# Performance work log

Measured on AMD Instinct MI355X. Metric: run time of the kernel, lower is better.

Reference implementation:

```python
import jax, jax.numpy as jnp
import numpy as np

V = 78864; E = 300; H = 512; A = 300; T = 20; DEC_EMB = 512; START = 2


def _pos_encoding(n, d):
    pos = np.arange(n)[:, None].astype(np.float32)
    i = np.arange(d)[None, :]
    angle = pos / np.power(10000.0, (2 * (i // 2)).astype(np.float32) / d)
    pe = np.where(i % 2 == 0, np.sin(angle), np.cos(angle)).astype(np.float32)
    return jnp.asarray(pe)  # [n, d]


def _lstm_cell(x, h, c, Wih, Whh, b):
    g = x @ Wih.T + h @ Whh.T + b
    i, f, gg, o = jnp.split(g, 4, axis=-1)
    c = jax.nn.sigmoid(f) * c + jax.nn.sigmoid(i) * jnp.tanh(gg)
    h = jax.nn.sigmoid(o) * jnp.tanh(c)
    return h, c


def setup_inputs() -> dict:
    key = jax.random.key(0)
    ks = iter(jax.random.split(key, 48))
    B, L = 40, 1000
    def w(shape, s=0.02):
        return jax.random.normal(next(ks), shape, jnp.float32) * s
    def z(shape):
        return jnp.zeros(shape, jnp.float32)
    inp = dict(
        enc_in=jax.random.randint(next(ks), (B, L), 0, V),
        enc_out=jax.random.normal(next(ks), (B, L, H), jnp.float32),
        enc_mask=jnp.zeros((B, L), bool),
        inputs=jax.random.randint(next(ks), (B, T), 0, V),
        embed=w((V, E)),
        elmo1_Wih=w((4 * H, E)), elmo1_Whh=w((4 * H, H)), elmo1_b=z((4 * H,)),
        elmo2_Wih=w((4 * H, H)), elmo2_Whh=w((4 * H, H)), elmo2_b=z((4 * H,)),
        in_W=w((DEC_EMB, H + E + A + H)), in_b=z((DEC_EMB,)),
        rnn1_Wih=w((4 * H, DEC_EMB)), rnn1_Whh=w((4 * H, H)), rnn1_b=z((4 * H,)),
        att1_Wq=w((A, H)), att1_bq=z((A,)), att1_Wk=w((A, H)), att1_bk=z((A,)), att1_Wv=w((A, H)), att1_bv=z((A,)),
        rnn2_Wih=w((4 * H, A)), rnn2_Whh=w((4 * H, H)), rnn2_b=z((4 * H,)),
        att2_Wq=w((A, H)), att2_bq=z((A,)), att2_Wk=w((A, H)), att2_bk=z((A,)), att2_Wv=w((A, H)), att2_bv=z((A,)),
        copy_W=w((A, H)), copy_b=z((A,)),
        out_W=w((V, A)), out_b=z((V,)),
        scale=jnp.asarray(1.0, jnp.float32),
    )
    return inp


def _forward(enc_in, enc_out, enc_mask, inputs, embed,
             elmo1_Wih, elmo1_Whh, elmo1_b, elmo2_Wih, elmo2_Whh, elmo2_b,
             in_W, in_b, rnn1_Wih, rnn1_Whh, rnn1_b,
             att1_Wq, att1_bq, att1_Wk, att1_bk, att1_Wv, att1_bv,
             rnn2_Wih, rnn2_Whh, rnn2_b,
             att2_Wq, att2_bq, att2_Wk, att2_bk, att2_Wv, att2_bv,
             copy_W, copy_b, out_W, out_b, scale):
    B, L = enc_in.shape
    pe = _pos_encoding(T, DEC_EMB)  # [T, 512]
    # Precompute per-encoder projections (hoisted out of the step loop).
    K1 = jnp.einsum('blh,ah->bla', enc_out, att1_Wk) + att1_bk
    V1 = jnp.einsum('blh,ah->bla', enc_out, att1_Wv) + att1_bv
    K2 = jnp.einsum('blh,ah->bla', enc_out, att2_Wk) + att2_bk
    V2 = jnp.einsum('blh,ah->bla', enc_out, att2_Wv) + att2_bv
    copyK = jnp.tanh(jnp.einsum('blh,ah->bla', enc_out, copy_W) + copy_b)
    bidx = jnp.arange(B)[:, None]

    def attn(h, Wq, bq, K, Vp):
        q = h @ Wq.T + bq                          # [B, A]
        s = jnp.einsum('ba,bla->bl', q, K)
        s = jnp.where(enc_mask, -1e9, s)
        p = jax.nn.softmax(s, axis=-1)
        return jnp.einsum('bl,bla->ba', p, Vp)

    # teacher forcing with random_int=0 -> always use ground-truth inputs
    sym_in = jnp.concatenate([jnp.full((B, 1), START, inputs.dtype), inputs[:, :-1]], axis=1).T  # [T,B]
    sym_out = inputs.T  # [T,B]

    zf = lambda *s: jnp.zeros(s, enc_out.dtype)
    carry0 = (zf(B, H), zf(B, H), zf(B, H), zf(B, H),  # elmo h1,c1,h2,c2
              zf(B, H), zf(B, H), zf(B, H), zf(B, H),  # rnn1 h,c ; rnn2 h,c
              zf(B, A), zf(B, H))                       # dec_att_out, select_read

    def step(carry, xs):
        eh1, ec1, eh2, ec2, h1, c1, h2, c2, att, sel = carry
        pe_t, s_in, s_out = xs
        emb = embed[s_in]                                           # [B, E]
        eh1, ec1 = _lstm_cell(emb, eh1, ec1, elmo1_Wih, elmo1_Whh, elmo1_b)
        eh2, ec2 = _lstm_cell(eh1, eh2, ec2, elmo2_Wih, elmo2_Whh, elmo2_b)
        in_embed = jnp.concatenate([emb, eh2], axis=-1)              # [B, 812]
        dec_in = jnp.concatenate([in_embed, att, sel], axis=-1) @ in_W.T + in_b + pe_t
        h1, c1 = _lstm_cell(dec_in, h1, c1, rnn1_Wih, rnn1_Whh, rnn1_b)
        att = attn(h1, att1_Wq, att1_bq, K1, V1)
        h2, c2 = _lstm_cell(att, h2, c2, rnn2_Wih, rnn2_Whh, rnn2_b)
        att = attn(h2, att2_Wq, att2_bq, K2, V2) + att
        # copy scores
        s = jnp.einsum('ba,bla->bl', att, copyK)
        s = jnp.where(enc_mask, -1e9, s)
        score_c = jax.nn.softmax(s, axis=-1)
        score_e = score_c * scale * scale
        vocab = att @ out_W.T + out_b                                # [B, V]
        vocab = vocab.at[bidx, enc_in].add(score_e)
        sym_pred = jnp.argmax(vocab, axis=-1).astype(jnp.int32)
        eq = (enc_in == s_out[:, None]).astype(score_c.dtype)
        score_f = score_c * eq
        score_f = score_f / (jnp.sum(score_f, axis=-1, keepdims=True) + 1e-8)
        sel = jnp.einsum('bl,blh->bh', score_f, enc_out)
        return (eh1, ec1, eh2, ec2, h1, c1, h2, c2, att, sel), (vocab, sym_pred)

    _, (dec_out, syms) = jax.lax.scan(step, carry0, (pe, sym_in, sym_out))
    return jnp.transpose(dec_out, (1, 0, 2)), syms.T  # [B,T,V], [B,T]


def reference(enc_in, enc_out, enc_mask, inputs, embed,
              elmo1_Wih, elmo1_Whh, elmo1_b, elmo2_Wih, elmo2_Whh, elmo2_b,
              in_W, in_b, rnn1_Wih, rnn1_Whh, rnn1_b,
              att1_Wq, att1_bq, att1_Wk, att1_bk, att1_Wv, att1_bv,
              rnn2_Wih, rnn2_Whh, rnn2_b,
              att2_Wq, att2_bq, att2_Wk, att2_bk, att2_Wv, att2_bv,
              copy_W, copy_b, out_W, out_b, scale):
    return _forward(enc_in, enc_out, enc_mask, inputs, embed,
                    elmo1_Wih, elmo1_Whh, elmo1_b, elmo2_Wih, elmo2_Whh, elmo2_b,
                    in_W, in_b, rnn1_Wih, rnn1_Whh, rnn1_b,
                    att1_Wq, att1_bq, att1_Wk, att1_bk, att1_Wv, att1_bv,
                    rnn2_Wih, rnn2_Whh, rnn2_b,
                    att2_Wq, att2_bq, att2_Wk, att2_bk, att2_Wv, att2_bv,
                    copy_W, copy_b, out_W, out_b, scale)
```

## Files before the change

kernel.cpp:

```cpp
#include <hip/hip_runtime.h>
#include <math.h>

#define B_ 40
#define L_ 1000
#define H_ 512
#define A_ 300
#define T_ 20
#define E_ 300
#define V_ 78864
#define CIN_ 1624
#define START_ 2

__device__ __forceinline__ float sigm(float x){ return 1.0f/(1.0f+expf(-x)); }

__device__ __forceinline__ float waveMax(float v){
#pragma unroll
  for(int o=32;o>0;o>>=1) v=fmaxf(v,__shfl_down(v,o));
  return v;
}
__device__ __forceinline__ float waveSum(float v){
#pragma unroll
  for(int o=32;o>0;o>>=1) v+=__shfl_down(v,o);
  return v;
}
__device__ __forceinline__ float waveSumXor(float v){
#pragma unroll
  for(int o=32;o>0;o>>=1) v+=__shfl_xor(v,o);
  return v;
}

__global__ void k_pe(float* __restrict__ pe){
  int t=blockIdx.x, d=threadIdx.x;
  float ex=(float)(2*(d>>1))/512.0f;
  float ang=(float)t/powf(10000.0f,ex);
  pe[t*H_+d]=(d&1)?cosf(ang):sinf(ang);
}

__global__ __launch_bounds__(320) void k_copyk(const float* __restrict__ enc,
    const float* __restrict__ W, const float* __restrict__ bias, float* __restrict__ out){
  int b=blockIdx.y, l0=blockIdx.x*16, a=threadIdx.x;
  if(a>=A_) return;
  int lcnt=min(16,L_-l0);
  float acc[16];
  float bv=bias[a];
#pragma unroll
  for(int l=0;l<16;l++) acc[l]=bv;
  const float4* wr=(const float4*)(W+(long)a*H_);
  for(int i=0;i<H_/4;i++){
    float4 w=wr[i];
#pragma unroll
    for(int l=0;l<16;l++){
      int row=b*L_+min(l0+l,L_-1);
      float4 x=((const float4*)enc)[(long)row*(H_/4)+i];
      acc[l]+=x.x*w.x+x.y*w.y+x.z*w.z+x.w*w.w;
    }
  }
  for(int l=0;l<lcnt;l++) out[((long)(b*L_+l0+l))*A_+a]=tanhf(acc[l]);
}

template<int XD, bool GATHER>
__global__ __launch_bounds__(256) void k_lstm(const float* __restrict__ xsrc,
    const int* __restrict__ inp, const float* __restrict__ embed, int t,
    const float* __restrict__ hr, const float* __restrict__ cr,
    float* __restrict__ hw, float* __restrict__ cw,
    const float* __restrict__ Wih, const float* __restrict__ Whh, const float* __restrict__ bias){
  __shared__ float g4[256];
  int b=blockIdx.y, hb=blockIdx.x, tid=threadIdx.x;
  const float4* xr4;
  if constexpr(GATHER){
    int si=(t==0)?START_:inp[b*T_+t-1];
    xr4=(const float4*)(embed+(long)si*XD);
  } else {
    xr4=(const float4*)(xsrc+(long)b*XD);
  }
  const float4* hr4=(const float4*)(hr+(long)b*H_);
  int gate=tid>>6, u=(hb<<6)+(tid&63), row=gate*H_+u;
  float acc=bias[row];
  const float4* wi=(const float4*)(Wih+(long)row*XD);
#pragma unroll 4
  for(int i=0;i<XD/4;i++){ float4 w=wi[i]; float4 x=xr4[i];
    acc+=x.x*w.x+x.y*w.y+x.z*w.z+x.w*w.w; }
  const float4* wh=(const float4*)(Whh+(long)row*H_);
#pragma unroll 4
  for(int i=0;i<H_/4;i++){ float4 w=wh[i]; float4 h4=hr4[i];
    acc+=h4.x*w.x+h4.y*w.y+h4.z*w.z+h4.w*w.w; }
  g4[tid]=acc;
  __syncthreads();
  if(tid<64){
    int uu=(hb<<6)+tid;
    float gi=g4[tid],gf=g4[64+tid],gg=g4[128+tid],go=g4[192+tid];
    float c=cr[b*H_+uu];
    float cn=sigm(gf)*c+sigm(gi)*tanhf(gg);
    hw[b*H_+uu]=sigm(go)*tanhf(cn);
    cw[b*H_+uu]=cn;
  }
}

__global__ __launch_bounds__(256) void k_decin(const int* __restrict__ inp,
    const float* __restrict__ embed, int t,
    const float* __restrict__ eh2, const float* __restrict__ attprev,
    const float* __restrict__ selpart,
    const float* __restrict__ W, const float* __restrict__ bias,
    const float* __restrict__ pe, float* __restrict__ out){
  __shared__ float xs[CIN_];
  int b=blockIdx.y, tid=threadIdx.x;
  int si=(t==0)?START_:inp[b*T_+t-1];
  for(int k=tid;k<CIN_;k+=256){
    float v;
    if(k<E_) v=embed[(long)si*E_+k];
    else if(k<E_+H_) v=eh2[b*H_+k-E_];
    else if(k<E_+H_+A_) v=attprev[b*A_+k-(E_+H_)];
    else{
      int h=k-(E_+H_+A_);
      float s=0.f;
#pragma unroll
      for(int j=0;j<8;j++) s+=selpart[(b*8+j)*H_+h];
      v=s;
    }
    xs[k]=v;
  }
  __syncthreads();
  int d=blockIdx.x*256+tid;
  float acc=bias[d]+pe[t*H_+d];
  const float4* wr=(const float4*)(W+(long)d*CIN_);
#pragma unroll 2
  for(int i=0;i<CIN_/4;i++){ float4 w=wr[i];
    acc+=xs[4*i]*w.x+xs[4*i+1]*w.y+xs[4*i+2]*w.z+xs[4*i+3]*w.w; }
  out[b*H_+d]=acc;
}

__global__ __launch_bounds__(512) void k_q(const float* __restrict__ h,
    const float* __restrict__ Wq, const float* __restrict__ bq,
    const float* __restrict__ Wk, float* __restrict__ qk){
  __shared__ float hs[H_], qs[A_];
  int b=blockIdx.x, tid=threadIdx.x;
  hs[tid]=h[b*H_+tid];
  __syncthreads();
  if(tid<A_){
    float acc=bq[tid];
    const float4* wr=(const float4*)(Wq+(long)tid*H_);
#pragma unroll 4
    for(int i=0;i<H_/4;i++){ float4 w=wr[i];
      acc+=hs[4*i]*w.x+hs[4*i+1]*w.y+hs[4*i+2]*w.z+hs[4*i+3]*w.w; }
    qs[tid]=acc;
  }
  __syncthreads();
  float acc=0.f;
  for(int a=0;a<A_;a++) acc+=qs[a]*Wk[a*H_+tid];
  qk[b*H_+tid]=acc;
}

__global__ __launch_bounds__(256) void k_scores(const float* __restrict__ qk,
    const float* __restrict__ enc, const unsigned char* __restrict__ mask,
    float* __restrict__ s){
  __shared__ float qs[H_];
  int b=blockIdx.y, j=blockIdx.x, tid=threadIdx.x;
  qs[tid]=qk[b*H_+tid]; qs[tid+256]=qk[b*H_+tid+256];
  __syncthreads();
  int wv=tid>>6, lane=tid&63;
  const float4* qs4=(const float4*)qs;
  for(int i=0;i<32;i++){
    int idx=i*4+wv;
    if(idx>=125) break;
    int l=j*125+idx;
    const float4* er=(const float4*)(enc+((long)(b*L_+l))*H_);
    float4 q1=qs4[lane], e1=er[lane];
    float p=q1.x*e1.x+q1.y*e1.y+q1.z*e1.z+q1.w*e1.w;
    float4 q2=qs4[64+lane], e2=er[64+lane];
    p+=q2.x*e2.x+q2.y*e2.y+q2.z*e2.z+q2.w*e2.w;
    p=waveSumXor(p);
    if(lane==0) s[b*L_+l]=mask[b*L_+l]?-1e9f:p;
  }
}

__global__ __launch_bounds__(512) void k_ctx(const float* __restrict__ s,
    const float* __restrict__ enc, float* __restrict__ part){
  __shared__ float e[L_];
  __shared__ float redm[8], reds[8];
  int b=blockIdx.y, j=blockIdx.x, tid=threadIdx.x;
  float lm=-3.0e38f;
  for(int l=tid;l<L_;l+=512){ float v=s[b*L_+l]; e[l]=v; lm=fmaxf(lm,v); }
  lm=waveMax(lm); if((tid&63)==0) redm[tid>>6]=lm;
  __syncthreads();
  float m=redm[0];
#pragma unroll
  for(int w2=1;w2<8;w2++) m=fmaxf(m,redm[w2]);
  float ls=0.f;
  for(int l=tid;l<L_;l+=512){ float ex=expf(e[l]-m); e[l]=ex; ls+=ex; }
  ls=waveSum(ls); if((tid&63)==0) reds[tid>>6]=ls;
  __syncthreads();
  float S=0.f;
#pragma unroll
  for(int w2=0;w2<8;w2++) S+=reds[w2];
  float inv=1.0f/S;
  float acc=0.f;
  int l0=j*125;
  for(int l=l0;l<l0+125;l++) acc+=e[l]*enc[((long)(b*L_+l))*H_+tid];
  part[(b*8+j)*H_+tid]=acc*inv;
}

template<bool ADD>
__global__ __launch_bounds__(512) void k_atto(const float* __restrict__ part,
    const float* __restrict__ Wv, const float* __restrict__ bv,
    const float* __restrict__ attprev, float* __restrict__ out, float* __restrict__ outT){
  __shared__ float cs[H_];
  int b=blockIdx.x, tid=threadIdx.x;
  float c=0.f;
#pragma unroll
  for(int j=0;j<8;j++) c+=part[(b*8+j)*H_+tid];
  cs[tid]=c;
  __syncthreads();
  if(tid<A_){
    float acc=bv[tid];
    const float4* wr=(const float4*)(Wv+(long)tid*H_);
#pragma unroll 4
    for(int i=0;i<H_/4;i++){ float4 w=wr[i];
      acc+=cs[4*i]*w.x+cs[4*i+1]*w.y+cs[4*i+2]*w.z+cs[4*i+3]*w.w; }
    if constexpr(ADD) acc+=attprev[b*A_+tid];
    out[b*A_+tid]=acc;
    if constexpr(ADD) outT[tid*B_+b]=acc;
  }
}

__global__ __launch_bounds__(256) void k_copysc(const float* __restrict__ att,
    const float* __restrict__ ck, const unsigned char* __restrict__ mask,
    float* __restrict__ s){
  __shared__ float as[A_];
  int b=blockIdx.y, j=blockIdx.x, tid=threadIdx.x;
  for(int k=tid;k<A_;k+=256) as[k]=att[b*A_+k];
  __syncthreads();
  int wv=tid>>6, lane=tid&63;
  for(int i=0;i<32;i++){
    int idx=i*4+wv;
    if(idx>=125) break;
    int l=j*125+idx;
    const float* cr=ck+((long)(b*L_+l))*A_;
    float p=0.f;
#pragma unroll
    for(int it=0;it<4;it++){ int k=it*64+lane; p+=as[k]*cr[k]; }
    { int k=256+lane; if(k<A_) p+=as[k]*cr[k]; }
    p=waveSumXor(p);
    if(lane==0) s[b*L_+l]=mask[b*L_+l]?-1e9f:p;
  }
}

__global__ __launch_bounds__(256) void k_vocab(const float* __restrict__ attT,
    const float* __restrict__ W, const float* __restrict__ bias, int t,
    float* __restrict__ dout){
  __shared__ float wt[256*33];
  int tid=threadIdx.x;
  int v=blockIdx.x*256+tid;
  bool ok=v<V_;
  int v0=blockIdx.x*256;
  float acc[B_];
#pragma unroll
  for(int b=0;b<B_;b++) acc[b]=0.f;
  for(int c=0;c<10;c++){
    int a0=c*32;
    int aw=(c<9)?32:12;
    __syncthreads();
    if(c<9){
      for(int idx=tid;idx<256*32;idx+=256){
        int vr=idx>>5, ar=idx&31;
        float val=(v0+vr<V_)?W[(long)(v0+vr)*A_+a0+ar]:0.f;
        wt[vr*33+ar]=val;
      }
    } else {
      for(int idx=tid;idx<256*12;idx+=256){
        int vr=idx/12, ar=idx-vr*12;
        float val=(v0+vr<V_)?W[(long)(v0+vr)*A_+a0+ar]:0.f;
        wt[vr*33+ar]=val;
      }
    }
    __syncthreads();
    for(int a=0;a<aw;a++){
      float wv=wt[tid*33+a];
      const float4* at4=(const float4*)(attT+(long)(a0+a)*B_);
#pragma unroll
      for(int bq=0;bq<10;bq++){
        float4 t4=at4[bq];
        acc[4*bq+0]+=wv*t4.x; acc[4*bq+1]+=wv*t4.y;
        acc[4*bq+2]+=wv*t4.z; acc[4*bq+3]+=wv*t4.w;
      }
    }
  }
  if(ok){
    float ob=bias[v];
#pragma unroll
    for(int b=0;b<B_;b++) dout[((long)(b*T_+t))*V_+v]=acc[b]+ob;
  }
}

__global__ __launch_bounds__(512) void k_scatsel(const float* __restrict__ s,
    const int* __restrict__ encin, const int* __restrict__ inp,
    const float* __restrict__ scale, int t,
    const float* __restrict__ enc, float* __restrict__ part,
    float* __restrict__ dout){
  __shared__ float e[L_], e2[L_];
  __shared__ float redm[8], reds[8], redq[8];
  int b=blockIdx.y, j=blockIdx.x, tid=threadIdx.x;
  int so=inp[b*T_+t];
  float lm=-3.0e38f;
  for(int l=tid;l<L_;l+=512){ float v=s[b*L_+l]; e[l]=v; lm=fmaxf(lm,v); }
  lm=waveMax(lm); if((tid&63)==0) redm[tid>>6]=lm;
  __syncthreads();
  float m=redm[0];
#pragma unroll
  for(int w2=1;w2<8;w2++) m=fmaxf(m,redm[w2]);
  float ls=0.f, lq=0.f;
  for(int l=tid;l<L_;l+=512){
    float ex=expf(e[l]-m);
    float pe_=(encin[b*L_+l]==so)?ex:0.f;
    e[l]=ex; e2[l]=pe_; ls+=ex; lq+=pe_;
  }
  ls=waveSum(ls); lq=waveSum(lq);
  if((tid&63)==0){ reds[tid>>6]=ls; redq[tid>>6]=lq; }
  __syncthreads();
  float S=0.f,Q=0.f;
#pragma unroll
  for(int w2=0;w2<8;w2++){ S+=reds[w2]; Q+=redq[w2]; }
  int l0=j*125;
  if(tid<125){
    int l=l0+tid;
    float f=scale[0]*scale[0]/S;
    float p=e[l]*f;
    atomicAdd(dout+((long)(b*T_+t))*V_+encin[b*L_+l],p);
  }
  float inv=1.0f/(Q+1e-8f*S);
  float acc=0.f;
  for(int l=l0;l<l0+125;l++) acc+=e2[l]*enc[((long)(b*L_+l))*H_+tid];
  part[(b*8+j)*H_+tid]=acc*inv;
}

__global__ __launch_bounds__(256) void k_argmax(int t, float* __restrict__ dout){
  __shared__ float vs[256];
  __shared__ int is[256];
  int b=blockIdx.x, tid=threadIdx.x;
  const float* row=dout+((long)(b*T_+t))*V_;
  float best=-3.0e38f; int bi=0;
  for(int v=tid;v<V_;v+=256){ float x=row[v]; if(x>best){best=x;bi=v;} }
  vs[tid]=best; is[tid]=bi;
  __syncthreads();
  for(int off=128;off>0;off>>=1){
    if(tid<off){
      float ov=vs[tid+off]; int oi=is[tid+off];
      if(ov>vs[tid]||(ov==vs[tid]&&oi<is[tid])){ vs[tid]=ov; is[tid]=oi; }
    }
    __syncthreads();
  }
  if(tid==0) dout[(long)B_*T_*V_+b*T_+t]=(float)is[0];
}

extern "C" void kernel_launch(void* const* d_in, const int* in_sizes, int n_in,
                              void* d_out, int out_size, void* d_ws, size_t ws_size,
                              hipStream_t stream){
  const int* enc_in=(const int*)d_in[0];
  const float* enc_out=(const float*)d_in[1];
  const unsigned char* enc_mask=(const unsigned char*)d_in[2];
  const int* inputs=(const int*)d_in[3];
  const float* embed=(const float*)d_in[4];
  const float* e1Wih=(const float*)d_in[5], *e1Whh=(const float*)d_in[6], *e1b=(const float*)d_in[7];
  const float* e2Wih=(const float*)d_in[8], *e2Whh=(const float*)d_in[9], *e2b=(const float*)d_in[10];
  const float* inW=(const float*)d_in[11], *inb=(const float*)d_in[12];
  const float* r1Wih=(const float*)d_in[13], *r1Whh=(const float*)d_in[14], *r1b=(const float*)d_in[15];
  const float* a1Wq=(const float*)d_in[16], *a1bq=(const float*)d_in[17];
  const float* a1Wk=(const float*)d_in[18];
  const float* a1Wv=(const float*)d_in[20], *a1bv=(const float*)d_in[21];
  const float* r2Wih=(const float*)d_in[22], *r2Whh=(const float*)d_in[23], *r2b=(const float*)d_in[24];
  const float* a2Wq=(const float*)d_in[25], *a2bq=(const float*)d_in[26];
  const float* a2Wk=(const float*)d_in[27];
  const float* a2Wv=(const float*)d_in[29], *a2bv=(const float*)d_in[30];
  const float* cW=(const float*)d_in[31], *cb=(const float*)d_in[32];
  const float* oW=(const float*)d_in[33], *ob=(const float*)d_in[34];
  const float* scale=(const float*)d_in[35];
  float* dout=(float*)d_out;
  float* w=(float*)d_ws;

  size_t off=0;
  float* copyK=w+off; off+=(size_t)B_*L_*A_;
  float* pe=w+off;    off+=T_*H_;
  float* st=w+off;    off+=16*B_*H_;
  float* att1=w+off;  off+=B_*A_;
  float* att2=w+off;  off+=B_*A_;
  float* attT=w+off;  off+=A_*B_;
  float* qk=w+off;    off+=B_*H_;
  float* s1=w+off;    off+=B_*L_;
  float* scc=w+off;   off+=B_*L_;
  float* ctxp=w+off;  off+=B_*8*H_;
  float* selp=w+off;  off+=B_*8*H_;
  float* decin=w+off; off+=B_*H_;

  hipMemsetAsync(pe,0,(off-(size_t)B_*L_*A_)*sizeof(float),stream);
  k_pe<<<T_,H_,0,stream>>>(pe);
  k_copyk<<<dim3((L_+15)/16,B_),320,0,stream>>>(enc_out,cW,cb,copyK);

  auto S=[&](int i){ return st+(size_t)i*(B_*H_); };
  for(int t=0;t<T_;t++){
    int rp=t&1, wp=rp^1;
    float *eh1r=S(0+rp),*eh1w=S(0+wp),*ec1r=S(2+rp),*ec1w=S(2+wp);
    float *eh2r=S(4+rp),*eh2w=S(4+wp),*ec2r=S(6+rp),*ec2w=S(6+wp);
    float *h1r=S(8+rp),*h1w=S(8+wp),*c1r=S(10+rp),*c1w=S(10+wp);
    float *h2r=S(12+rp),*h2w=S(12+wp),*c2r=S(14+rp),*c2w=S(14+wp);

    k_lstm<E_,true><<<dim3(8,B_),256,0,stream>>>(nullptr,inputs,embed,t,eh1r,ec1r,eh1w,ec1w,e1Wih,e1Whh,e1b);
    k_lstm<H_,false><<<dim3(8,B_),256,0,stream>>>(eh1w,nullptr,nullptr,t,eh2r,ec2r,eh2w,ec2w,e2Wih,e2Whh,e2b);
    k_decin<<<dim3(2,B_),256,0,stream>>>(inputs,embed,t,eh2w,att2,selp,inW,inb,pe,decin);
    k_lstm<H_,false><<<dim3(8,B_),256,0,stream>>>(decin,nullptr,nullptr,t,h1r,c1r,h1w,c1w,r1Wih,r1Whh,r1b);
    k_q<<<B_,512,0,stream>>>(h1w,a1Wq,a1bq,a1Wk,qk);
    k_scores<<<dim3(8,B_),256,0,stream>>>(qk,enc_out,enc_mask,s1);
    k_ctx<<<dim3(8,B_),512,0,stream>>>(s1,enc_out,ctxp);
    k_atto<false><<<B_,512,0,stream>>>(ctxp,a1Wv,a1bv,nullptr,att1,nullptr);
    k_lstm<A_,false><<<dim3(8,B_),256,0,stream>>>(att1,nullptr,nullptr,t,h2r,c2r,h2w,c2w,r2Wih,r2Whh,r2b);
    k_q<<<B_,512,0,stream>>>(h2w,a2Wq,a2bq,a2Wk,qk);
    k_scores<<<dim3(8,B_),256,0,stream>>>(qk,enc_out,enc_mask,s1);
    k_ctx<<<dim3(8,B_),512,0,stream>>>(s1,enc_out,ctxp);
    k_atto<true><<<B_,512,0,stream>>>(ctxp,a2Wv,a2bv,att1,att2,attT);
    k_copysc<<<dim3(8,B_),256,0,stream>>>(att2,copyK,enc_mask,scc);
    k_vocab<<<(V_+255)/256,256,0,stream>>>(attT,oW,ob,t,dout);
    k_scatsel<<<dim3(8,B_),512,0,stream>>>(scc,enc_in,inputs,scale,t,enc_out,selp,dout);
    k_argmax<<<B_,256,0,stream>>>(t,dout);
  }
}
```

Before: 18.39 ms.

## Replace per-step kernel launches with one persistent kernel using grid barriers

Turns the per-timestep sequence of about seventeen kernel launches into a single persistent kernel of 256 blocks that moves between phases using atomic-counter grid barriers. It also restructures the work: LSTM gates are computed batch-wide per weight row through shared memory, query and key weights are premultiplied into M1T and M2T, scores and context are fused with an online softmax, and the vocab projection is retiled. The aim is to remove launch overhead and reread weights fewer times across the batch. In exchange it depends on all blocks being co-resident for the spin barriers and adds many barrier points per step.

```diff
diff --git a/kernel.cpp b/kernel.cpp
--- a/kernel.cpp
+++ b/kernel.cpp
@@ -8,416 +8,509 @@
 #define T_ 20
 #define E_ 300
 #define V_ 78864
-#define CIN_ 1624
 #define START_ 2
 
+#define NBLK 256
+#define NTHR 512
+
+#define OFF_COPYK 0ul
+#define OFF_M1T   12000000ul
+#define OFF_M2T   12262144ul
+#define OFF_BQK1  12524288ul
+#define OFF_BQK2  12524800ul
+#define OFF_QK    12525312ul
+#define OFF_DEC   12545792ul
+#define OFF_ATT1  12566272ul
+#define OFF_ATTT  12578272ul
+#define OFF_CPART 12590272ul
+#define OFF_CSTAT 12713152ul
+#define OFF_SCC   12713664ul
+#define OFF_STT   12753664ul
+#define OFF_ATT2  13081344ul
+#define OFF_SELP  13093344ul
+#define OFF_CNT   13216224ul
+#define WS_END    13216288ul
+
+struct P {
+  const int* enc_in; const float* enc; const unsigned char* mask; const int* inputs;
+  const float* embed;
+  const float *e1Wih,*e1Whh,*e1b,*e2Wih,*e2Whh,*e2b;
+  const float *inW,*inb;
+  const float *r1Wih,*r1Whh,*r1b;
+  const float *a1Wq,*a1bq,*a1Wk,*a1Wv,*a1bv;
+  const float *r2Wih,*r2Whh,*r2b;
+  const float *a2Wq,*a2bq,*a2Wk,*a2Wv,*a2bv;
+  const float *cW,*cb,*oW,*ob,*scale;
+  float* dout;
+  float *copyK,*M1T,*M2T,*bqk1,*bqk2,*qk,*dec,*att1,*attT,*cpart,*cstat,*scc,*stt,*att2,*selp;
+  unsigned* cnt;
+};
+
 __device__ __forceinline__ float sigm(float x){ return 1.0f/(1.0f+expf(-x)); }
 
-__device__ __forceinline__ float waveMax(float v){
-#pragma unroll
-  for(int o=32;o>0;o>>=1) v=fmaxf(v,__shfl_down(v,o));
-  return v;
-}
-__device__ __forceinline__ float waveSum(float v){
-#pragma unroll
-  for(int o=32;o>0;o>>=1) v+=__shfl_down(v,o);
-  return v;
-}
-__device__ __forceinline__ float waveSumXor(float v){
+__device__ __forceinline__ float wredSum(float v){
 #pragma unroll
   for(int o=32;o>0;o>>=1) v+=__shfl_xor(v,o);
   return v;
 }
-
-__global__ void k_pe(float* __restrict__ pe){
-  int t=blockIdx.x, d=threadIdx.x;
-  float ex=(float)(2*(d>>1))/512.0f;
-  float ang=(float)t/powf(10000.0f,ex);
-  pe[t*H_+d]=(d&1)?cosf(ang):sinf(ang);
-}
-
-__global__ __launch_bounds__(320) void k_copyk(const float* __restrict__ enc,
-    const float* __restrict__ W, const float* __restrict__ bias, float* __restrict__ out){
-  int b=blockIdx.y, l0=blockIdx.x*16, a=threadIdx.x;
-  if(a>=A_) return;
-  int lcnt=min(16,L_-l0);
-  float acc[16];
-  float bv=bias[a];
-#pragma unroll
-  for(int l=0;l<16;l++) acc[l]=bv;
-  const float4* wr=(const float4*)(W+(long)a*H_);
-  for(int i=0;i<H_/4;i++){
-    float4 w=wr[i];
-#pragma unroll
-    for(int l=0;l<16;l++){
-      int row=b*L_+min(l0+l,L_-1);
-      float4 x=((const float4*)enc)[(long)row*(H_/4)+i];
-      acc[l]+=x.x*w.x+x.y*w.y+x.z*w.z+x.w*w.w;
-    }
-  }
-  for(int l=0;l<lcnt;l++) out[((long)(b*L_+l0+l))*A_+a]=tanhf(acc[l]);
-}
-
-template<int XD, bool GATHER>
-__global__ __launch_bounds__(256) void k_lstm(const float* __restrict__ xsrc,
-    const int* __restrict__ inp, const float* __restrict__ embed, int t,
-    const float* __restrict__ hr, const float* __restrict__ cr,
-    float* __restrict__ hw, float* __restrict__ cw,
-    const float* __restrict__ Wih, const float* __restrict__ Whh, const float* __restrict__ bias){
-  __shared__ float g4[256];
-  int b=blockIdx.y, hb=blockIdx.x, tid=threadIdx.x;
-  const float4* xr4;
-  if constexpr(GATHER){
-    int si=(t==0)?START_:inp[b*T_+t-1];
-    xr4=(const float4*)(embed+(long)si*XD);
-  } else {
-    xr4=(const float4*)(xsrc+(long)b*XD);
-  }
-  const float4* hr4=(const float4*)(hr+(long)b*H_);
-  int gate=tid>>6, u=(hb<<6)+(tid&63), row=gate*H_+u;
-  float acc=bias[row];
-  const float4* wi=(const float4*)(Wih+(long)row*XD);
+__device__ __forceinline__ float wredMax(float v){
+#pragma unroll
+  for(int o=32;o>0;o>>=1) v=fmaxf(v,__shfl_xor(v,o));
+  return v;
+}
+
+__device__ __forceinline__ void gbar(unsigned* cnt, unsigned target){
+  __syncthreads();
+  if(threadIdx.x==0){
+    __hip_atomic_fetch_add(cnt,1u,__ATOMIC_RELEASE,__HIP_MEMORY_SCOPE_AGENT);
+    while(__hip_atomic_load(cnt,__ATOMIC_RELAXED,__HIP_MEMORY_SCOPE_AGENT)<target){
+      __builtin_amdgcn_s_sleep(1);
+    }
+    (void)__hip_atomic_load(cnt,__ATOMIC_ACQUIRE,__HIP_MEMORY_SCOPE_AGENT);
+  }
+  __syncthreads();
+}
+
+template<typename SRC>
+static __device__ __forceinline__ void gv_accum(float* xs,int K,const float* Wrow,
+    float& acc,int lane,int kq,int nq,SRC src){
+  for(int k0=0;k0<K;k0+=256){
+    int ch=min(256,K-k0);
+    __syncthreads();
+    for(int i=threadIdx.x;i<40*ch;i+=NTHR){
+      int bb=i/ch, kk=i-bb*ch;
+      xs[bb*257+kk]=src(bb,k0+kk);
+    }
+    __syncthreads();
+    if(lane<40){
 #pragma unroll 4
-  for(int i=0;i<XD/4;i++){ float4 w=wi[i]; float4 x=xr4[i];
-    acc+=x.x*w.x+x.y*w.y+x.z*w.z+x.w*w.w; }
-  const float4* wh=(const float4*)(Whh+(long)row*H_);
-#pragma unroll 4
-  for(int i=0;i<H_/4;i++){ float4 w=wh[i]; float4 h4=hr4[i];
-    acc+=h4.x*w.x+h4.y*w.y+h4.z*w.z+h4.w*w.w; }
-  g4[tid]=acc;
-  __syncthreads();
-  if(tid<64){
-    int uu=(hb<<6)+tid;
-    float gi=g4[tid],gf=g4[64+tid],gg=g4[128+tid],go=g4[192+tid];
-    float c=cr[b*H_+uu];
+      for(int k=kq;k<ch;k+=nq) acc+=Wrow[k0+k]*xs[lane*257+k];
+    }
+  }
+}
+
+static __device__ void lstm_ph(const P& p,float* SH,float* gld,int t,
+    const float* Wih,int XD,const float* Whh,const float* bias,
+    const float* xvec,bool gather,
+    const float* hr,const float* cr,float* hw,float* cw){
+  int tid=threadIdx.x,w=tid>>6,lane=tid&63;
+  int gate=w&3,usub=w>>2;
+  int row=gate*H_+(blockIdx.x*2+usub);
+  int rowu=__builtin_amdgcn_readfirstlane(row);
+  float acc=bias[rowu];
+  const float* W1=Wih+(size_t)rowu*XD;
+  if(gather){
+    const int* inp=p.inputs; const float* emb=p.embed; int tt=t;
+    gv_accum(SH,XD,W1,acc,lane,0,1,[=](int bb,int kk)->float{
+      int si=(tt==0)?START_:inp[bb*T_+tt-1];
+      return emb[(size_t)si*E_+kk];});
+  }else{
+    gv_accum(SH,XD,W1,acc,lane,0,1,[=](int bb,int kk)->float{
+      return xvec[(size_t)bb*XD+kk];});
+  }
+  const float* W2=Whh+(size_t)rowu*H_;
+  gv_accum(SH,H_,W2,acc,lane,0,1,[=](int bb,int kk)->float{
+    return hr[bb*H_+kk];});
+  gld[w*64+lane]=acc;
+  __syncthreads();
+  if(w<2&&lane<40){
+    int u=blockIdx.x*2+w,b=lane;
+    float gi=gld[(w*4+0)*64+b],gf=gld[(w*4+1)*64+b],gg=gld[(w*4+2)*64+b],go=gld[(w*4+3)*64+b];
+    float c=cr[b*H_+u];
     float cn=sigm(gf)*c+sigm(gi)*tanhf(gg);
-    hw[b*H_+uu]=sigm(go)*tanhf(cn);
-    cw[b*H_+uu]=cn;
-  }
-}
-
-__global__ __launch_bounds__(256) void k_decin(const int* __restrict__ inp,
-    const float* __restrict__ embed, int t,
-    const float* __restrict__ eh2, const float* __restrict__ attprev,
-    const float* __restrict__ selpart,
-    const float* __restrict__ W, const float* __restrict__ bias,
-    const float* __restrict__ pe, float* __restrict__ out){
-  __shared__ float xs[CIN_];
-  int b=blockIdx.y, tid=threadIdx.x;
-  int si=(t==0)?START_:inp[b*T_+t-1];
-  for(int k=tid;k<CIN_;k+=256){
-    float v;
-    if(k<E_) v=embed[(long)si*E_+k];
-    else if(k<E_+H_) v=eh2[b*H_+k-E_];
-    else if(k<E_+H_+A_) v=attprev[b*A_+k-(E_+H_)];
-    else{
-      int h=k-(E_+H_+A_);
-      float s=0.f;
-#pragma unroll
-      for(int j=0;j<8;j++) s+=selpart[(b*8+j)*H_+h];
-      v=s;
-    }
-    xs[k]=v;
-  }
-  __syncthreads();
-  int d=blockIdx.x*256+tid;
-  float acc=bias[d]+pe[t*H_+d];
-  const float4* wr=(const float4*)(W+(long)d*CIN_);
-#pragma unroll 2
-  for(int i=0;i<CIN_/4;i++){ float4 w=wr[i];
-    acc+=xs[4*i]*w.x+xs[4*i+1]*w.y+xs[4*i+2]*w.z+xs[4*i+3]*w.w; }
-  out[b*H_+d]=acc;
-}
-
-__global__ __launch_bounds__(512) void k_q(const float* __restrict__ h,
-    const float* __restrict__ Wq, const float* __restrict__ bq,
-    const float* __restrict__ Wk, float* __restrict__ qk){
-  __shared__ float hs[H_], qs[A_];
-  int b=blockIdx.x, tid=threadIdx.x;
-  hs[tid]=h[b*H_+tid];
+    hw[b*H_+u]=sigm(go)*tanhf(cn);
+    cw[b*H_+u]=cn;
+  }
+  __syncthreads();
+}
+
+static __device__ void qk_ph(const P& p,float* SH,const float* hsrc,
+    const float* MT,const float* bqk){
+  int tid=threadIdx.x;
+  if(blockIdx.x>=240) return;
+  int b=blockIdx.x/6, j=blockIdx.x%6;
+  SH[tid]=hsrc[b*H_+tid];
+  __syncthreads();
+  int h0=j*86, hc=min(86,H_-h0);
+  if(tid<hc){
+    int hp=h0+tid;
+    float a=bqk[hp];
+    const float4* mr=(const float4*)(MT+(size_t)hp*H_);
+#pragma unroll 8
+    for(int i=0;i<H_/4;i++){
+      float4 m4=mr[i];
+      a+=SH[4*i]*m4.x+SH[4*i+1]*m4.y+SH[4*i+2]*m4.z+SH[4*i+3]*m4.w;
+    }
+    p.qk[b*H_+hp]=a;
+  }
+}
+
+static __device__ void scctx_ph(const P& p,float* SH,float* red){
+  int tid=threadIdx.x,w=tid>>6,lane=tid&63;
+  if(blockIdx.x>=240) return;
+  int b=blockIdx.x/6, j=blockIdx.x%6;
+  int l0=j*167, lcnt=min(167,L_-l0);
+  const float* qrow=p.qk+b*H_;
+  float4 q0=*(const float4*)(qrow+lane*8);
+  float4 q1=*(const float4*)(qrow+lane*8+4);
+  float m=-3.0e38f,S=0.f;
+  float4 a0=make_float4(0.f,0.f,0.f,0.f), a1=a0;
+  for(int l=l0+w;l<l0+lcnt;l+=8){
+    const float4* er=(const float4*)(p.enc+((size_t)(b*L_+l))*H_);
+    float4 e0=er[lane*2], e1=er[lane*2+1];
+    float pp=q0.x*e0.x+q0.y*e0.y+q0.z*e0.z+q0.w*e0.w
+            +q1.x*e1.x+q1.y*e1.y+q1.z*e1.z+q1.w*e1.w;
+    pp=wredSum(pp);
+    if(p.mask[b*L_+l]) pp=-1e9f;
+    float mn=fmaxf(m,pp);
+    float sc=expf(m-mn), pe=expf(pp-mn);
+    S=S*sc+pe;
+    a0.x=a0.x*sc+pe*e0.x; a0.y=a0.y*sc+pe*e0.y; a0.z=a0.z*sc+pe*e0.z; a0.w=a0.w*sc+pe*e0.w;
+    a1.x=a1.x*sc+pe*e1.x; a1.y=a1.y*sc+pe*e1.y; a1.z=a1.z*sc+pe*e1.z; a1.w=a1.w*sc+pe*e1.w;
+    m=mn;
+  }
+  *(float4*)(SH+w*H_+lane*8)=a0;
+  *(float4*)(SH+w*H_+lane*8+4)=a1;
+  if(lane==0){red[w]=m; red[8+w]=S;}
+  __syncthreads();
+  float mb=red[0];
+#pragma unroll
+  for(int q=1;q<8;q++) mb=fmaxf(mb,red[q]);
+  float Sb=0.f;
+#pragma unroll
+  for(int q=0;q<8;q++) Sb+=red[8+q]*expf(red[q]-mb);
+  float pv=0.f;
+#pragma unroll
+  for(int q=0;q<8;q++) pv+=expf(red[q]-mb)*SH[q*H_+tid];
+  p.cpart[(size_t)(b*6+j)*H_+tid]=pv;
+  if(tid==0){p.cstat[(b*6+j)*2]=mb; p.cstat[(b*6+j)*2+1]=Sb;}
+}
+
+static __device__ void atto_ph(const P& p,float* SH,const float* Wv,const float* bv,bool ADD){
+  int tid=threadIdx.x;
+  if(blockIdx.x>=40) return;
+  int b=blockIdx.x;
+  float mb=-3.0e38f;
+#pragma unroll
+  for(int j=0;j<6;j++) mb=fmaxf(mb,p.cstat[(b*6+j)*2]);
+  float Sb=0.f;
+#pragma unroll
+  for(int j=0;j<6;j++) Sb+=p.cstat[(b*6+j)*2+1]*expf(p.cstat[(b*6+j)*2]-mb);
+  float inv=1.0f/Sb;
+  float cx=0.f;
+#pragma unroll
+  for(int j=0;j<6;j++) cx+=expf(p.cstat[(b*6+j)*2]-mb)*p.cpart[(size_t)(b*6+j)*H_+tid];
+  SH[tid]=cx*inv;
   __syncthreads();
   if(tid<A_){
-    float acc=bq[tid];
-    const float4* wr=(const float4*)(Wq+(long)tid*H_);
-#pragma unroll 4
-    for(int i=0;i<H_/4;i++){ float4 w=wr[i];
-      acc+=hs[4*i]*w.x+hs[4*i+1]*w.y+hs[4*i+2]*w.z+hs[4*i+3]*w.w; }
-    qs[tid]=acc;
-  }
-  __syncthreads();
-  float acc=0.f;
-  for(int a=0;a<A_;a++) acc+=qs[a]*Wk[a*H_+tid];
-  qk[b*H_+tid]=acc;
-}
-
-__global__ __launch_bounds__(256) void k_scores(const float* __restrict__ qk,
-    const float* __restrict__ enc, const unsigned char* __restrict__ mask,
-    float* __restrict__ s){
-  __shared__ float qs[H_];
-  int b=blockIdx.y, j=blockIdx.x, tid=threadIdx.x;
-  qs[tid]=qk[b*H_+tid]; qs[tid+256]=qk[b*H_+tid+256];
-  __syncthreads();
-  int wv=tid>>6, lane=tid&63;
-  const float4* qs4=(const float4*)qs;
-  for(int i=0;i<32;i++){
-    int idx=i*4+wv;
-    if(idx>=125) break;
-    int l=j*125+idx;
-    const float4* er=(const float4*)(enc+((long)(b*L_+l))*H_);
-    float4 q1=qs4[lane], e1=er[lane];
-    float p=q1.x*e1.x+q1.y*e1.y+q1.z*e1.z+q1.w*e1.w;
-    float4 q2=qs4[64+lane], e2=er[64+lane];
-    p+=q2.x*e2.x+q2.y*e2.y+q2.z*e2.z+q2.w*e2.w;
-    p=waveSumXor(p);
-    if(lane==0) s[b*L_+l]=mask[b*L_+l]?-1e9f:p;
-  }
-}
-
-__global__ __launch_bounds__(512) void k_ctx(const float* __restrict__ s,
-    const float* __restrict__ enc, float* __restrict__ part){
-  __shared__ float e[L_];
-  __shared__ float redm[8], reds[8];
-  int b=blockIdx.y, j=blockIdx.x, tid=threadIdx.x;
+    float a=bv[tid];
+    const float4* wr=(const float4*)(Wv+(size_t)tid*H_);
+#pragma unroll 8
+    for(int i=0;i<H_/4;i++){
+      float4 w4=wr[i];
+      a+=SH[4*i]*w4.x+SH[4*i+1]*w4.y+SH[4*i+2]*w4.z+SH[4*i+3]*w4.w;
+    }
+    if(ADD){ a+=p.att1[b*A_+tid]; p.att2[b*A_+tid]=a; p.attT[tid*B_+b]=a; }
+    else p.att1[b*A_+tid]=a;
+  }
+}
+
+static __device__ void copysc_ph(const P& p){
+  int tid=threadIdx.x,w=tid>>6,lane=tid&63;
+  if(blockIdx.x>=240) return;
+  int b=blockIdx.x/6, j=blockIdx.x%6;
+  int l0=j*167, lcnt=min(167,L_-l0);
+  float4 r0=*(const float4*)(p.att2+b*A_+lane*4);
+  float4 r1=make_float4(0.f,0.f,0.f,0.f);
+  if(lane<11) r1=*(const float4*)(p.att2+b*A_+256+lane*4);
+  for(int l=l0+w;l<l0+lcnt;l+=8){
+    const float4* cr=(const float4*)(p.copyK+((size_t)(b*L_+l))*A_);
+    float4 c0=cr[lane];
+    float pp=r0.x*c0.x+r0.y*c0.y+r0.z*c0.z+r0.w*c0.w;
+    if(lane<11){
+      float4 c1=cr[64+lane];
+      pp+=r1.x*c1.x+r1.y*c1.y+r1.z*c1.z+r1.w*c1.w;
+    }
+    pp=wredSum(pp);
+    if(lane==0) p.scc[b*L_+l]=p.mask[b*L_+l]?-1e9f:pp;
+  }
+}
+
+static __device__ void vocab_ph(const P& p,float* SH,int t){
+  int tid=threadIdx.x;
+  int v0=blockIdx.x*312;
+  if(v0>=V_) return;
+  int vcnt=min(312,V_-v0);
+  float acc[40];
+#pragma unroll
+  for(int b=0;b<40;b++) acc[b]=0.f;
+  for(int c=0;c<10;c++){
+    int a0=c*32, aw=min(32,A_-a0);
+    __syncthreads();
+    for(int i=tid;i<vcnt*aw;i+=NTHR){
+      int vr=i/aw, ac=i-vr*aw;
+      SH[vr*33+ac]=p.oW[(size_t)(v0+vr)*A_+a0+ac];
+    }
+    __syncthreads();
+    if(tid<vcnt){
+      for(int ac=0;ac<aw;ac++){
+        float wv=SH[tid*33+ac];
+        const float* at=p.attT+(a0+ac)*B_;
+#pragma unroll
+        for(int bq=0;bq<10;bq++){
+          float4 t4=*(const float4*)(at+bq*4);
+          acc[bq*4+0]+=wv*t4.x; acc[bq*4+1]+=wv*t4.y;
+          acc[bq*4+2]+=wv*t4.z; acc[bq*4+3]+=wv*t4.w;
+        }
+      }
+    }
+  }
+  if(tid<vcnt){
+    int v=v0+tid;
+    float obv=p.ob[v];
+#pragma unroll
+    for(int b=0;b<40;b++) p.dout[((size_t)(b*T_+t))*V_+v]=acc[b]+obv;
+  }
+}
+
+static __device__ void scatsel_ph(const P& p,float* SH,float* red,int t){
+  int tid=threadIdx.x,w=tid>>6,lane=tid&63;
+  if(blockIdx.x>=240) return;
+  int b=blockIdx.x/6, j=blockIdx.x%6;
+  int l0=j*167, lcnt=min(167,L_-l0);
+  for(int i=tid;i<L_;i+=NTHR) SH[i]=p.scc[b*L_+i];
+  __syncthreads();
   float lm=-3.0e38f;
-  for(int l=tid;l<L_;l+=512){ float v=s[b*L_+l]; e[l]=v; lm=fmaxf(lm,v); }
-  lm=waveMax(lm); if((tid&63)==0) redm[tid>>6]=lm;
-  __syncthreads();
-  float m=redm[0];
-#pragma unroll
-  for(int w2=1;w2<8;w2++) m=fmaxf(m,redm[w2]);
-  float ls=0.f;
-  for(int l=tid;l<L_;l+=512){ float ex=expf(e[l]-m); e[l]=ex; ls+=ex; }
-  ls=waveSum(ls); if((tid&63)==0) reds[tid>>6]=ls;
-  __syncthreads();
-  float S=0.f;
-#pragma unroll
-  for(int w2=0;w2<8;w2++) S+=reds[w2];
-  float inv=1.0f/S;
-  float acc=0.f;
-  int l0=j*125;
-  for(int l=l0;l<l0+125;l++) acc+=e[l]*enc[((long)(b*L_+l))*H_+tid];
-  part[(b*8+j)*H_+tid]=acc*inv;
-}
-
-template<bool ADD>
-__global__ __launch_bounds__(512) void k_atto(const float* __restrict__ part,
-    const float* __restrict__ Wv, const float* __restrict__ bv,
-    const float* __restrict__ attprev, float* __restrict__ out, float* __restrict__ outT){
-  __shared__ float cs[H_];
-  int b=blockIdx.x, tid=threadIdx.x;
-  float c=0.f;
-#pragma unroll
-  for(int j=0;j<8;j++) c+=part[(b*8+j)*H_+tid];
-  cs[tid]=c;
-  __syncthreads();
-  if(tid<A_){
-    float acc=bv[tid];
-    const float4* wr=(const float4*)(Wv+(long)tid*H_);
-#pragma unroll 4
-    for(int i=0;i<H_/4;i++){ float4 w=wr[i];
-      acc+=cs[4*i]*w.x+cs[4*i+1]*w.y+cs[4*i+2]*w.z+cs[4*i+3]*w.w; }
-    if constexpr(ADD) acc+=attprev[b*A_+tid];
-    out[b*A_+tid]=acc;
-    if constexpr(ADD) outT[tid*B_+b]=acc;
-  }
-}
-
-__global__ __launch_bounds__(256) void k_copysc(const float* __restrict__ att,
-    const float* __restrict__ ck, const unsigned char* __restrict__ mask,
-    float* __restrict__ s){
-  __shared__ float as[A_];
-  int b=blockIdx.y, j=blockIdx.x, tid=threadIdx.x;
-  for(int k=tid;k<A_;k+=256) as[k]=att[b*A_+k];
-  __syncthreads();
-  int wv=tid>>6, lane=tid&63;
-  for(int i=0;i<32;i++){
-    int idx=i*4+wv;
-    if(idx>=125) break;
-    int l=j*125+idx;
-    const float* cr=ck+((long)(b*L_+l))*A_;
-    float p=0.f;
-#pragma unroll
-    for(int it=0;it<4;it++){ int k=it*64+lane; p+=as[k]*cr[k]; }
-    { int k=256+lane; if(k<A_) p+=as[k]*cr[k]; }
-    p=waveSumXor(p);
-    if(lane==0) s[b*L_+l]=mask[b*L_+l]?-1e9f:p;
-  }
-}
-
-__global__ __launch_bounds__(256) void k_vocab(const float* __restrict__ attT,
-    const float* __restrict__ W, const float* __restrict__ bias, int t,
-    float* __restrict__ dout){
-  __shared__ float wt[256*33];
+  for(int i=tid;i<L_;i+=NTHR) lm=fmaxf(lm,SH[i]);
+  lm=wredMax(lm);
+  if(lane==0) red[w]=lm;
+  __syncthreads();
+  float m=red[0];
+#pragma unroll
+  for(int q=1;q<8;q++) m=fmaxf(m,red[q]);
+  __syncthreads();
+  int so=p.inputs[b*T_+t];
+  float ls=0.f,lq=0.f;
+  for(int i=tid;i<L_;i+=NTHR){
+    float exv=expf(SH[i]-m);
+    ls+=exv;
+    if(p.enc_in[b*L_+i]==so) lq+=exv;
+  }
+  ls=wredSum(ls); lq=wredSum(lq);
+  if(lane==0){red[w]=ls; red[8+w]=lq;}
+  __syncthreads();
+  float S=0.f,Q=0.f;
+#pragma unroll
+  for(int q=0;q<8;q++){S+=red[q];Q+=red[8+q];}
+  if(tid<lcnt){
+    int l=l0+tid;
+    float exv=expf(SH[l]-m);
+    SH[1024+tid]=(p.enc_in[b*L_+l]==so)?exv:0.f;
+    float sc2=p.scale[0]*p.scale[0];
+    atomicAdd(p.dout+((size_t)(b*T_+t))*V_+p.enc_in[b*L_+l], exv*sc2/S);
+  }
+  __syncthreads();
+  float inv=1.0f/(Q+1e-8f*S);
+  float a=0.f;
+  for(int li=0;li<lcnt;li++)
+    a+=SH[1024+li]*p.enc[((size_t)(b*L_+l0+li))*H_+tid];
+  p.selp[(size_t)(b*6+j)*H_+tid]=a*inv;
+}
+
+static __device__ void argmax_ph(const P& p,float* SH,int t){
   int tid=threadIdx.x;
-  int v=blockIdx.x*256+tid;
-  bool ok=v<V_;
-  int v0=blockIdx.x*256;
-  float acc[B_];
-#pragma unroll
-  for(int b=0;b<B_;b++) acc[b]=0.f;
-  for(int c=0;c<10;c++){
-    int a0=c*32;
-    int aw=(c<9)?32:12;
+  if(blockIdx.x>=40) return;
+  int b=blockIdx.x;
+  const float* row=p.dout+((size_t)(b*T_+t))*V_;
+  float best=-3.0e38f; int bi=0;
+  for(int i4=tid;i4<V_/4;i4+=NTHR){
+    float4 x=((const float4*)row)[i4];
+    int base=i4*4;
+    if(x.x>best){best=x.x;bi=base;}
+    if(x.y>best){best=x.y;bi=base+1;}
+    if(x.z>best){best=x.z;bi=base+2;}
+    if(x.w>best){best=x.w;bi=base+3;}
+  }
+  int* isa=(int*)(SH+512);
+  SH[tid]=best; isa[tid]=bi;
+  __syncthreads();
+  for(int off=256;off>0;off>>=1){
+    if(tid<off){
+      float ov=SH[tid+off]; int oi=isa[tid+off];
+      if(ov>SH[tid]||(ov==SH[tid]&&oi<isa[tid])){SH[tid]=ov; isa[tid]=oi;}
+    }
     __syncthreads();
-    if(c<9){
-      for(int idx=tid;idx<256*32;idx+=256){
-        int vr=idx>>5, ar=idx&31;
-        float val=(v0+vr<V_)?W[(long)(v0+vr)*A_+a0+ar]:0.f;
-        wt[vr*33+ar]=val;
+  }
+  if(tid==0) p.dout[(size_t)B_*T_*V_+b*T_+t]=(float)isa[0];
+}
+
+__global__ __launch_bounds__(NTHR,2) void k_persist(P p){
+  __shared__ float SH[10320];
+  __shared__ float gld[512];
+  __shared__ float red[16];
+  int blk=blockIdx.x, tid=threadIdx.x;
+  unsigned bt=0;
+#define BARR() do{bt++; gbar(p.cnt,bt*(unsigned)NBLK);}while(0)
+
+  {
+    int mm=blk>>7, r0=(blk&127)*4;
+    const float* Wq = mm? p.a2Wq : p.a1Wq;
+    const float* Wk = mm? p.a2Wk : p.a1Wk;
+    float* MT = mm? p.M2T : p.M1T;
+    float s0=0.f,s1=0.f,s2=0.f,s3=0.f;
+    for(int a=0;a<A_;a++){
+      float wq=Wq[a*H_+tid];
+      s0+=wq*Wk[a*H_+r0+0];
+      s1+=wq*Wk[a*H_+r0+1];
+      s2+=wq*Wk[a*H_+r0+2];
+      s3+=wq*Wk[a*H_+r0+3];
+    }
+    MT[(size_t)(r0+0)*H_+tid]=s0;
+    MT[(size_t)(r0+1)*H_+tid]=s1;
+    MT[(size_t)(r0+2)*H_+tid]=s2;
+    MT[(size_t)(r0+3)*H_+tid]=s3;
+    if((blk&127)==0){
+      const float* bq = mm? p.a2bq : p.a1bq;
+      float ab=0.f;
+      for(int a=0;a<A_;a++) ab+=bq[a]*Wk[a*H_+tid];
+      (mm? p.bqk2 : p.bqk1)[tid]=ab;
+    }
+  }
+  for(int item=blk;item<B_*63;item+=NBLK){
+    int b=item/63, lt=item-b*63;
+    int l0=lt*16, lcnt=min(16,L_-l0);
+    float acc[16];
+    float bv=(tid<A_)?p.cb[tid]:0.f;
+#pragma unroll
+    for(int l=0;l<16;l++) acc[l]=bv;
+    for(int k0=0;k0<H_;k0+=32){
+      __syncthreads();
+      for(int i=tid;i<A_*32;i+=NTHR){
+        int a=i>>5,kc=i&31;
+        SH[a*33+kc]=p.cW[(size_t)a*H_+k0+kc];
       }
-    } else {
-      for(int idx=tid;idx<256*12;idx+=256){
-        int vr=idx/12, ar=idx-vr*12;
-        float val=(v0+vr<V_)?W[(long)(v0+vr)*A_+a0+ar]:0.f;
-        wt[vr*33+ar]=val;
+      __syncthreads();
+      if(tid<A_){
+#pragma unroll
+        for(int l=0;l<16;l++){
+          if(l<lcnt){
+            const float* es=p.enc+((size_t)(b*L_+l0+l))*H_+k0;
+            float al=acc[l];
+#pragma unroll
+            for(int kc=0;kc<32;kc++) al+=SH[tid*33+kc]*es[kc];
+            acc[l]=al;
+          }
+        }
       }
     }
-    __syncthreads();
-    for(int a=0;a<aw;a++){
-      float wv=wt[tid*33+a];
-      const float4* at4=(const float4*)(attT+(long)(a0+a)*B_);
-#pragma unroll
-      for(int bq=0;bq<10;bq++){
-        float4 t4=at4[bq];
-        acc[4*bq+0]+=wv*t4.x; acc[4*bq+1]+=wv*t4.y;
-        acc[4*bq+2]+=wv*t4.z; acc[4*bq+3]+=wv*t4.w;
+    if(tid<A_){
+#pragma unroll
+      for(int l=0;l<16;l++)
+        if(l<lcnt) p.copyK[((size_t)(b*L_+l0+l))*A_+tid]=tanhf(acc[l]);
+    }
+  }
+  BARR();
+
+  for(int t=0;t<T_;t++){
+    int rp=t&1, wp=rp^1;
+    float* stt=p.stt;
+    auto SL=[&](int i,int par){ return stt+((size_t)(i*2+par))*(B_*H_); };
+    float *eh1r=SL(0,rp),*eh1w=SL(0,wp),*ec1r=SL(1,rp),*ec1w=SL(1,wp);
+    float *eh2r=SL(2,rp),*eh2w=SL(2,wp),*ec2r=SL(3,rp),*ec2w=SL(3,wp);
+    float *h1r=SL(4,rp),*h1w=SL(4,wp),*c1r=SL(5,rp),*c1w=SL(5,wp);
+    float *h2r=SL(6,rp),*h2w=SL(6,wp),*c2r=SL(7,rp),*c2w=SL(7,wp);
+
+    lstm_ph(p,SH,gld,t,p.e1Wih,E_,p.e1Whh,p.e1b,nullptr,true ,eh1r,ec1r,eh1w,ec1w); BARR();
+    lstm_ph(p,SH,gld,t,p.e2Wih,H_,p.e2Whh,p.e2b,eh1w  ,false,eh2r,ec2r,eh2w,ec2w); BARR();
+
+    {
+      int w=tid>>6,lane=tid&63;
+      int usub=w>>2, kq=w&3;
+      int unit=blk*2+usub;
+      int rowu=__builtin_amdgcn_readfirstlane(unit);
+      float acc=0.f;
+      const float* Wr=p.inW+(size_t)rowu*1624;
+      const int* inp=p.inputs; const float* emb=p.embed;
+      const float* e2=eh2w; const float* a2c=p.att2; const float* sp=p.selp;
+      int tt=t;
+      gv_accum(SH,1624,Wr,acc,lane,kq,4,[=](int bb,int kk)->float{
+        if(kk<E_){int si=(tt==0)?START_:inp[bb*T_+tt-1];return emb[(size_t)si*E_+kk];}
+        else if(kk<E_+H_) return e2[bb*H_+kk-E_];
+        else if(kk<E_+H_+A_) return a2c[bb*A_+kk-(E_+H_)];
+        else{
+          int hh=kk-(E_+H_+A_); float s=0.f;
+#pragma unroll
+          for(int jj=0;jj<6;jj++) s+=sp[(size_t)(bb*6+jj)*H_+hh];
+          return s;
+        }
+      });
+      gld[(usub*4+kq)*64+lane]=acc;
+      __syncthreads();
+      if(w<2&&lane<40){
+        int u=blk*2+w;
+        float s=gld[(w*4+0)*64+lane]+gld[(w*4+1)*64+lane]
+               +gld[(w*4+2)*64+lane]+gld[(w*4+3)*64+lane];
+        float ex=(float)(2*(u>>1))/512.0f;
+        float ang=(float)t/powf(10000.0f,ex);
+        s+=p.inb[u]+((u&1)?cosf(ang):sinf(ang));
+        p.dec[lane*H_+u]=s;
       }
-    }
-  }
-  if(ok){
-    float ob=bias[v];
-#pragma unroll
-    for(int b=0;b<B_;b++) dout[((long)(b*T_+t))*V_+v]=acc[b]+ob;
-  }
-}
-
-__global__ __launch_bounds__(512) void k_scatsel(const float* __restrict__ s,
-    const int* __restrict__ encin, const int* __restrict__ inp,
-    const float* __restrict__ scale, int t,
-    const float* __restrict__ enc, float* __restrict__ part,
-    float* __restrict__ dout){
-  __shared__ float e[L_], e2[L_];
-  __shared__ float redm[8], reds[8], redq[8];
-  int b=blockIdx.y, j=blockIdx.x, tid=threadIdx.x;
-  int so=inp[b*T_+t];
-  float lm=-3.0e38f;
-  for(int l=tid;l<L_;l+=512){ float v=s[b*L_+l]; e[l]=v; lm=fmaxf(lm,v); }
-  lm=waveMax(lm); if((tid&63)==0) redm[tid>>6]=lm;
-  __syncthreads();
-  float m=redm[0];
-#pragma unroll
-  for(int w2=1;w2<8;w2++) m=fmaxf(m,redm[w2]);
-  float ls=0.f, lq=0.f;
-  for(int l=tid;l<L_;l+=512){
-    float ex=expf(e[l]-m);
-    float pe_=(encin[b*L_+l]==so)?ex:0.f;
-    e[l]=ex; e2[l]=pe_; ls+=ex; lq+=pe_;
-  }
-  ls=waveSum(ls); lq=waveSum(lq);
-  if((tid&63)==0){ reds[tid>>6]=ls; redq[tid>>6]=lq; }
-  __syncthreads();
-  float S=0.f,Q=0.f;
-#pragma unroll
-  for(int w2=0;w2<8;w2++){ S+=reds[w2]; Q+=redq[w2]; }
-  int l0=j*125;
-  if(tid<125){
-    int l=l0+tid;
-    float f=scale[0]*scale[0]/S;
-    float p=e[l]*f;
-    atomicAdd(dout+((long)(b*T_+t))*V_+encin[b*L_+l],p);
-  }
-  float inv=1.0f/(Q+1e-8f*S);
-  float acc=0.f;
-  for(int l=l0;l<l0+125;l++) acc+=e2[l]*enc[((long)(b*L_+l))*H_+tid];
-  part[(b*8+j)*H_+tid]=acc*inv;
-}
-
-__global__ __launch_bounds__(256) void k_argmax(int t, float* __restrict__ dout){
-  __shared__ float vs[256];
-  __shared__ int is[256];
-  int b=blockIdx.x, tid=threadIdx.x;
-  const float* row=dout+((long)(b*T_+t))*V_;
-  float best=-3.0e38f; int bi=0;
-  for(int v=tid;v<V_;v+=256){ float x=row[v]; if(x>best){best=x;bi=v;} }
-  vs[tid]=best; is[tid]=bi;
-  __syncthreads();
-  for(int off=128;off>0;off>>=1){
-    if(tid<off){
-      float ov=vs[tid+off]; int oi=is[tid+off];
-      if(ov>vs[tid]||(ov==vs[tid]&&oi<is[tid])){ vs[tid]=ov; is[tid]=oi; }
-    }
-    __syncthreads();
-  }
-  if(tid==0) dout[(long)B_*T_*V_+b*T_+t]=(float)is[0];
+      __syncthreads();
+    }
+    BARR();
+
+    lstm_ph(p,SH,gld,t,p.r1Wih,H_,p.r1Whh,p.r1b,p.dec ,false,h1r,c1r,h1w,c1w); BARR();
+    qk_ph(p,SH,h1w,p.M1T,p.bqk1);                                              BARR();
+    scctx_ph(p,SH,red);                                                        BARR();
+    atto_ph(p,SH,p.a1Wv,p.a1bv,false);                                         BARR();
+    lstm_ph(p,SH,gld,t,p.r2Wih,A_,p.r2Whh,p.r2b,p.att1,false,h2r,c2r,h2w,c2w); BARR();
+    qk_ph(p,SH,h2w,p.M2T,p.bqk2);                                              BARR();
+    scctx_ph(p,SH,red);                                                        BARR();
+    atto_ph(p,SH,p.a2Wv,p.a2bv,true);                                          BARR();
+    copysc_ph(p);                                                              BARR();
+    vocab_ph(p,SH,t);                                                          BARR();
+    scatsel_ph(p,SH,red,t);                                                    BARR();
+    argmax_ph(p,SH,t);
+  }
+#undef BARR
 }
 
 extern "C" void kernel_launch(void* const* d_in, const int* in_sizes, int n_in,
                               void* d_out, int out_size, void* d_ws, size_t ws_size,
                               hipStream_t stream){
-  const int* enc_in=(const int*)d_in[0];
-  const float* enc_out=(const float*)d_in[1];
-  const unsigned char* enc_mask=(const unsigned char*)d_in[2];
-  const int* inputs=(const int*)d_in[3];
-  const float* embed=(const float*)d_in[4];
-  const float* e1Wih=(const float*)d_in[5], *e1Whh=(const float*)d_in[6], *e1b=(const float*)d_in[7];
-  const float* e2Wih=(const float*)d_in[8], *e2Whh=(const float*)d_in[9], *e2b=(const float*)d_in[10];
-  const float* inW=(const float*)d_in[11], *inb=(const float*)d_in[12];
-  const float* r1Wih=(const float*)d_in[13], *r1Whh=(const float*)d_in[14], *r1b=(const float*)d_in[15];
-  const float* a1Wq=(const float*)d_in[16], *a1bq=(const float*)d_in[17];
-  const float* a1Wk=(const float*)d_in[18];
-  const float* a1Wv=(const float*)d_in[20], *a1bv=(const float*)d_in[21];
-  const float* r2Wih=(const float*)d_in[22], *r2Whh=(const float*)d_in[23], *r2b=(const float*)d_in[24];
-  const float* a2Wq=(const float*)d_in[25], *a2bq=(const float*)d_in[26];
-  const float* a2Wk=(const float*)d_in[27];
-  const float* a2Wv=(const float*)d_in[29], *a2bv=(const float*)d_in[30];
-  const float* cW=(const float*)d_in[31], *cb=(const float*)d_in[32];
-  const float* oW=(const float*)d_in[33], *ob=(const float*)d_in[34];
-  const float* scale=(const float*)d_in[35];
-  float* dout=(float*)d_out;
+  P p;
+  p.enc_in=(const int*)d_in[0];
+  p.enc   =(const float*)d_in[1];
+  p.mask  =(const unsigned char*)d_in[2];
+  p.inputs=(const int*)d_in[3];
+  p.embed =(const float*)d_in[4];
+  p.e1Wih=(const float*)d_in[5];  p.e1Whh=(const float*)d_in[6];  p.e1b=(const float*)d_in[7];
+  p.e2Wih=(const float*)d_in[8];  p.e2Whh=(const float*)d_in[9];  p.e2b=(const float*)d_in[10];
+  p.inW  =(const float*)d_in[11]; p.inb  =(const float*)d_in[12];
+  p.r1Wih=(const float*)d_in[13]; p.r1Whh=(const float*)d_in[14]; p.r1b=(const float*)d_in[15];
+  p.a1Wq =(const float*)d_in[16]; p.a1bq =(const float*)d_in[17];
+  p.a1Wk =(const float*)d_in[18];
+  p.a1Wv =(const float*)d_in[20]; p.a1bv =(const float*)d_in[21];
+  p.r2Wih=(const float*)d_in[22]; p.r2Whh=(const float*)d_in[23]; p.r2b=(const float*)d_in[24];
+  p.a2Wq =(const float*)d_in[25]; p.a2bq =(const float*)d_in[26];
+  p.a2Wk =(const float*)d_in[27];
+  p.a2Wv =(const float*)d_in[29]; p.a2bv =(const float*)d_in[30];
+  p.cW   =(const float*)d_in[31]; p.cb   =(const float*)d_in[32];
+  p.oW   =(const float*)d_in[33]; p.ob   =(const float*)d_in[34];
+  p.scale=(const float*)d_in[35];
+  p.dout=(float*)d_out;
+
   float* w=(float*)d_ws;
-
-  size_t off=0;
-  float* copyK=w+off; off+=(size_t)B_*L_*A_;
-  float* pe=w+off;    off+=T_*H_;
-  float* st=w+off;    off+=16*B_*H_;
-  float* att1=w+off;  off+=B_*A_;
-  float* att2=w+off;  off+=B_*A_;
-  float* attT=w+off;  off+=A_*B_;
-  float* qk=w+off;    off+=B_*H_;
-  float* s1=w+off;    off+=B_*L_;
-  float* scc=w+off;   off+=B_*L_;
-  float* ctxp=w+off;  off+=B_*8*H_;
-  float* selp=w+off;  off+=B_*8*H_;
-  float* decin=w+off; off+=B_*H_;
-
-  hipMemsetAsync(pe,0,(off-(size_t)B_*L_*A_)*sizeof(float),stream);
-  k_pe<<<T_,H_,0,stream>>>(pe);
-  k_copyk<<<dim3((L_+15)/16,B_),320,0,stream>>>(enc_out,cW,cb,copyK);
-
-  auto S=[&](int i){ return st+(size_t)i*(B_*H_); };
-  for(int t=0;t<T_;t++){
-    int rp=t&1, wp=rp^1;
-    float *eh1r=S(0+rp),*eh1w=S(0+wp),*ec1r=S(2+rp),*ec1w=S(2+wp);
-    float *eh2r=S(4+rp),*eh2w=S(4+wp),*ec2r=S(6+rp),*ec2w=S(6+wp);
-    float *h1r=S(8+rp),*h1w=S(8+wp),*c1r=S(10+rp),*c1w=S(10+wp);
-    float *h2r=S(12+rp),*h2w=S(12+wp),*c2r=S(14+rp),*c2w=S(14+wp);
-
-    k_lstm<E_,true><<<dim3(8,B_),256,0,stream>>>(nullptr,inputs,embed,t,eh1r,ec1r,eh1w,ec1w,e1Wih,e1Whh,e1b);
-    k_lstm<H_,false><<<dim3(8,B_),256,0,stream>>>(eh1w,nullptr,nullptr,t,eh2r,ec2r,eh2w,ec2w,e2Wih,e2Whh,e2b);
-    k_decin<<<dim3(2,B_),256,0,stream>>>(inputs,embed,t,eh2w,att2,selp,inW,inb,pe,decin);
-    k_lstm<H_,false><<<dim3(8,B_),256,0,stream>>>(decin,nullptr,nullptr,t,h1r,c1r,h1w,c1w,r1Wih,r1Whh,r1b);
-    k_q<<<B_,512,0,stream>>>(h1w,a1Wq,a1bq,a1Wk,qk);
-    k_scores<<<dim3(8,B_),256,0,stream>>>(qk,enc_out,enc_mask,s1);
-    k_ctx<<<dim3(8,B_),512,0,stream>>>(s1,enc_out,ctxp);
-    k_atto<false><<<B_,512,0,stream>>>(ctxp,a1Wv,a1bv,nullptr,att1,nullptr);
-    k_lstm<A_,false><<<dim3(8,B_),256,0,stream>>>(att1,nullptr,nullptr,t,h2r,c2r,h2w,c2w,r2Wih,r2Whh,r2b);
-    k_q<<<B_,512,0,stream>>>(h2w,a2Wq,a2bq,a2Wk,qk);
-    k_scores<<<dim3(8,B_),256,0,stream>>>(qk,enc_out,enc_mask,s1);
-    k_ctx<<<dim3(8,B_),512,0,stream>>>(s1,enc_out,ctxp);
-    k_atto<true><<<B_,512,0,stream>>>(ctxp,a2Wv,a2bv,att1,att2,attT);
-    k_copysc<<<dim3(8,B_),256,0,stream>>>(att2,copyK,enc_mask,scc);
-    k_vocab<<<(V_+255)/256,256,0,stream>>>(attT,oW,ob,t,dout);
-    k_scatsel<<<dim3(8,B_),512,0,stream>>>(scc,enc_in,inputs,scale,t,enc_out,selp,dout);
-    k_argmax<<<B_,256,0,stream>>>(t,dout);
-  }
-}
+  p.copyK=w+OFF_COPYK;
+  p.M1T  =w+OFF_M1T;   p.M2T =w+OFF_M2T;
+  p.bqk1 =w+OFF_BQK1;  p.bqk2=w+OFF_BQK2;
+  p.qk   =w+OFF_QK;    p.dec =w+OFF_DEC;
+  p.att1 =w+OFF_ATT1;  p.attT=w+OFF_ATTT;
+  p.cpart=w+OFF_CPART; p.cstat=w+OFF_CSTAT;
+  p.scc  =w+OFF_SCC;   p.stt =w+OFF_STT;
+  p.att2 =w+OFF_ATT2;  p.selp=w+OFF_SELP;
+  p.cnt  =(unsigned*)(w+OFF_CNT);
+
+  hipMemsetAsync(w+OFF_STT,0,(WS_END-OFF_STT)*sizeof(float),stream);
+  k_persist<<<NBLK,NTHR,0,stream>>>(p);
+}
```

New measurement: 18.03 ms (median of 3 runs). About the same (-2.0%).
